# Performance work log

Measured on AMD Instinct MI355X. Metric: run time of the kernel, lower is better.

## Reference

```python
import jax, jax.numpy as jnp
import numpy as np

N_NODES = 50000
N_EDGES = 625000
D_IN, D_HID, D_OUT = 512, 128, 1


def gcn_conv(x, W, b, src, dst, n_nodes):
    """PyG GCNConv: add self-loops, symmetric D^-1/2 (A+I) D^-1/2 normalization.
    x: [N, d_in], W: [d_in, d_out], b: [d_out], src/dst: [E] int.
    """
    xw = x @ W  # [N, d_out] - linear before propagation (PyG order)
    # degree including self-loop
    deg = jax.ops.segment_sum(jnp.ones_like(src, dtype=xw.dtype), dst,
                              num_segments=n_nodes) + 1.0
    dinv = jax.lax.rsqrt(deg)  # [N]
    norm = dinv[src] * dinv[dst]  # [E]
    # neighbor aggregation (scatter-add over destination nodes)
    agg = jax.ops.segment_sum(xw[src] * norm[:, None], dst, num_segments=n_nodes)
    # self-loop contribution: norm_ii = dinv_i^2
    agg = agg + xw * (dinv * dinv)[:, None]
    return agg + b


def layer_norm(x, gamma, beta, eps=1e-5):
    mu = jnp.mean(x, axis=-1, keepdims=True)
    var = jnp.var(x, axis=-1, keepdims=True)
    return (x - mu) * jax.lax.rsqrt(var + eps) * gamma + beta


def setup_inputs() -> dict:
    key = jax.random.key(0)
    ks = jax.random.split(key, 12)
    x = jax.random.normal(ks[0], (N_NODES, D_IN), dtype=jnp.float32)
    edge_index = jax.random.randint(ks[1], (2, N_EDGES), 0, N_NODES, dtype=jnp.int64)

    def glorot(k, shape):
        lim = np.sqrt(6.0 / (shape[0] + shape[1]))
        return jax.random.uniform(k, shape, jnp.float32, -lim, lim)

    return {
        "x": x,
        "W1": glorot(ks[2], (D_IN, D_HID)), "b1": jnp.zeros((D_HID,), jnp.float32),
        "gamma1": jnp.ones((D_HID,), jnp.float32), "beta1": jnp.zeros((D_HID,), jnp.float32),
        "W2": glorot(ks[3], (D_HID, D_HID)), "b2": jnp.zeros((D_HID,), jnp.float32),
        "W3": glorot(ks[4], (D_HID, D_HID)), "b3": jnp.zeros((D_HID,), jnp.float32),
        "W4": glorot(ks[5], (D_HID, D_OUT)), "b4": jnp.zeros((D_OUT,), jnp.float32),
        "edge_index": edge_index,
    }


def reference(x, W1, b1, gamma1, beta1, W2, b2, W3, b3, W4, b4, edge_index):
    # eval mode: F.dropout(training=False) is identity
    src, dst = edge_index[0], edge_index[1]
    n = x.shape[0]
    h = jax.nn.relu(layer_norm(gcn_conv(x, W1, b1, src, dst, n), gamma1, beta1))
    h = jax.nn.relu(gcn_conv(h, W2, b2, src, dst, n))
    h = jax.nn.relu(gcn_conv(h, W3, b3, src, dst, n))
    h = gcn_conv(h, W4, b4, src, dst, n)
    return jnp.squeeze(h, axis=-1)  # [N]
```

## Files before the change

### kernel.cpp

```cpp
#include <hip/hip_runtime.h>
#include <hip/hip_bf16.h>
#include <cstdint>

#define D_IN 512
#define D_HID 128

typedef unsigned short u16;
typedef unsigned int u32;
typedef __attribute__((ext_vector_type(8))) short short8;
typedef __attribute__((ext_vector_type(4))) float f32x4;

__device__ __forceinline__ u16 f2bf(float f) {
    u32 u = __float_as_uint(f);
    u = (u + 0x7FFFu + ((u >> 16) & 1u)) >> 16;
    return (u16)u;
}
__device__ __forceinline__ float bfc(short x) {
    return __uint_as_float(((u32)(u16)x) << 16);
}

__global__ __launch_bounds__(256) void k_deg_int(const int* __restrict__ dst,
                                                 int* __restrict__ deg, int E) {
    int e = blockIdx.x * 256 + threadIdx.x;
    if (e < E) atomicAdd(&deg[dst[e]], 1);
}

__global__ __launch_bounds__(256) void k_scan_block(const int* __restrict__ deg,
                                                    int* __restrict__ rowptr,
                                                    int* __restrict__ bsum, int N) {
    __shared__ int sh[256];
    int i = blockIdx.x * 256 + threadIdx.x;
    int v = (i < N) ? deg[i] : 0;
    sh[threadIdx.x] = v;
    __syncthreads();
#pragma unroll
    for (int off = 1; off < 256; off <<= 1) {
        int t = (threadIdx.x >= off) ? sh[threadIdx.x - off] : 0;
        __syncthreads();
        sh[threadIdx.x] += t;
        __syncthreads();
    }
    int incl = sh[threadIdx.x];
    if (i < N) rowptr[i] = incl - v;
    if (threadIdx.x == 255) bsum[blockIdx.x] = incl;
}

__global__ __launch_bounds__(256) void k_apply_offset(int* __restrict__ rowptr,
                                                      const int* __restrict__ bsum,
                                                      int* __restrict__ deg_cursor,
                                                      float* __restrict__ dinv,
                                                      int N, int E, int P) {
    __shared__ int sh[256];
    int v = (threadIdx.x < P) ? bsum[threadIdx.x] : 0;
    sh[threadIdx.x] = v;
    __syncthreads();
#pragma unroll
    for (int off = 1; off < 256; off <<= 1) {
        int t = (threadIdx.x >= off) ? sh[threadIdx.x - off] : 0;
        __syncthreads();
        sh[threadIdx.x] += t;
        __syncthreads();
    }
    int boff = (blockIdx.x == 0) ? 0 : sh[blockIdx.x - 1];
    int i = blockIdx.x * 256 + threadIdx.x;
    if (i == 0) rowptr[N] = E;
    if (i >= N) return;
    int dv = deg_cursor[i];
    int rp = rowptr[i] + boff;
    rowptr[i] = rp;
    deg_cursor[i] = rp;
    dinv[i] = rsqrtf((float)dv + 1.0f);
}

__global__ __launch_bounds__(256) void k_fill_csr(const int* __restrict__ src,
                                                  const int* __restrict__ dst,
                                                  int* __restrict__ cursor,
                                                  int* __restrict__ csr, int E) {
    int e = blockIdx.x * 256 + threadIdx.x;
    if (e >= E) return;
    int pos = atomicAdd(&cursor[dst[e]], 1);
    csr[pos] = src[e];
}

__global__ __launch_bounds__(256) void k_wt_all(const float* __restrict__ W1,
                                                const float* __restrict__ W2,
                                                const float* __restrict__ W3,
                                                u16* __restrict__ WT1,
                                                u16* __restrict__ WT2,
                                                u16* __restrict__ WT3) {
    int t = blockIdx.x * 256 + threadIdx.x;
    if (t < 65536) {
        int c = t >> 9, k = t & 511;
        WT1[t] = f2bf(W1[(size_t)k * 128 + c]);
    } else if (t < 65536 + 16384) {
        int u = t - 65536;
        int c = u >> 7, k = u & 127;
        WT2[u] = f2bf(W2[(size_t)k * 128 + c]);
    } else if (t < 65536 + 32768) {
        int u = t - 65536 - 16384;
        int c = u >> 7, k = u & 127;
        WT3[u] = f2bf(W3[(size_t)k * 128 + c]);
    }
}

template <int K, typename TI>
__global__ __launch_bounds__(256) void k_gemm_mfma(const TI* __restrict__ X,
                                                   const u16* __restrict__ WT,
                                                   const float* __restrict__ dinv,
                                                   u16* __restrict__ Y, int N) {
    __shared__ u16 Xs[64 * 40];
    __shared__ u16 Ws[128 * 40];
    const int tid = threadIdx.x;
    const int wv = tid >> 6;
    const int lane = tid & 63;
    const int row0 = blockIdx.x * 64;
    const int rsel = lane & 15;
    const int kgrp = (lane >> 4) * 8;

    f32x4 acc[8];
#pragma unroll
    for (int c = 0; c < 8; ++c) acc[c] = (f32x4){0.f, 0.f, 0.f, 0.f};

    for (int k0 = 0; k0 < K; k0 += 32) {
        {
            int r = tid >> 2;
            int kk = (tid & 3) * 8;
            int row = row0 + r;
            if constexpr (sizeof(TI) == 4) {
                float v[8];
                if (row < N) {
                    float4 p0 = *(const float4*)&X[(size_t)row * K + k0 + kk];
                    float4 p1 = *(const float4*)&X[(size_t)row * K + k0 + kk + 4];
                    v[0] = p0.x; v[1] = p0.y; v[2] = p0.z; v[3] = p0.w;
                    v[4] = p1.x; v[5] = p1.y; v[6] = p1.z; v[7] = p1.w;
                } else {
#pragma unroll
                    for (int i = 0; i < 8; ++i) v[i] = 0.f;
                }
                union { u16 us[8]; short8 v8; } tmp;
#pragma unroll
                for (int i = 0; i < 8; ++i) tmp.us[i] = f2bf(v[i]);
                *(short8*)&Xs[r * 40 + kk] = tmp.v8;
            } else {
                short8 v8 = {};
                if (row < N) v8 = *(const short8*)&X[(size_t)row * K + k0 + kk];
                *(short8*)&Xs[r * 40 + kk] = v8;
            }
        }
        {
            int col = tid >> 1;
            int kh = (tid & 1) * 16;
            const u16* g = &WT[(size_t)col * K + k0 + kh];
            u16* d = &Ws[col * 40 + kh];
            *(short8*)d = *(const short8*)g;
            *(short8*)(d + 8) = *(const short8*)(g + 8);
        }
        __syncthreads();
        short8 a = *(const short8*)&Xs[(wv * 16 + rsel) * 40 + kgrp];
#pragma unroll
        for (int c = 0; c < 8; ++c) {
            short8 b = *(const short8*)&Ws[(c * 16 + rsel) * 40 + kgrp];
            acc[c] = __builtin_amdgcn_mfma_f32_16x16x32_bf16(a, b, acc[c], 0, 0, 0);
        }
        __syncthreads();
    }
#pragma unroll
    for (int r = 0; r < 4; ++r) {
        int row = row0 + wv * 16 + (lane >> 4) * 4 + r;
        if (row < N) {
            float ds = dinv[row];
#pragma unroll
            for (int c = 0; c < 8; ++c)
                Y[(size_t)row * 128 + c * 16 + rsel] = f2bf(acc[c][r] * ds);
        }
    }
}

#define GATHER_CORE(XW, rowptr, csr, node, q, es, a)                               \
    int beg = rowptr[node], end = rowptr[node + 1];                                \
    float a[8];                                                                    \
    _Pragma("unroll") for (int i = 0; i < 8; ++i) a[i] = 0.f;                      \
    {                                                                              \
        int j = beg + es;                                                          \
        for (; j + 12 < end; j += 16) {                                            \
            int s0 = csr[j], s1 = csr[j + 4], s2 = csr[j + 8], s3 = csr[j + 12];   \
            short8 r0 = *(const short8*)&XW[(size_t)s0 * 128 + q * 8];             \
            short8 r1 = *(const short8*)&XW[(size_t)s1 * 128 + q * 8];             \
            short8 r2 = *(const short8*)&XW[(size_t)s2 * 128 + q * 8];             \
            short8 r3 = *(const short8*)&XW[(size_t)s3 * 128 + q * 8];             \
            _Pragma("unroll") for (int i = 0; i < 8; ++i)                          \
                a[i] += (bfc(r0[i]) + bfc(r1[i])) + (bfc(r2[i]) + bfc(r3[i]));     \
        }                                                                          \
        if (j + 4 < end) {                                                         \
            int s0 = csr[j], s1 = csr[j + 4];                                      \
            short8 r0 = *(const short8*)&XW[(size_t)s0 * 128 + q * 8];             \
            short8 r1 = *(const short8*)&XW[(size_t)s1 * 128 + q * 8];             \
            _Pragma("unroll") for (int i = 0; i < 8; ++i)                          \
                a[i] += bfc(r0[i]) + bfc(r1[i]);                                   \
            j += 8;                                                                \
        }                                                                          \
        if (j < end) {                                                             \
            int s = csr[j];                                                        \
            short8 r = *(const short8*)&XW[(size_t)s * 128 + q * 8];               \
            _Pragma("unroll") for (int i = 0; i < 8; ++i) a[i] += bfc(r[i]);       \
        }                                                                          \
    }                                                                              \
    _Pragma("unroll") for (int i = 0; i < 8; ++i) {                                \
        a[i] += __shfl_xor(a[i], 16);                                              \
        a[i] += __shfl_xor(a[i], 32);                                              \
    }

__global__ __launch_bounds__(256) void k_gather_ln_relu(const u16* __restrict__ XW,
                                                        const int* __restrict__ rowptr,
                                                        const int* __restrict__ csr,
                                                        const float* __restrict__ dinv,
                                                        const float* __restrict__ b,
                                                        const float* __restrict__ gamma,
                                                        const float* __restrict__ beta,
                                                        u16* __restrict__ H, int N) {
    int node = blockIdx.x * 4 + (threadIdx.x >> 6);
    int lane = threadIdx.x & 63;
    int q = lane & 15;
    int es = lane >> 4;
    if (node >= N) return;
    float di = dinv[node];
    GATHER_CORE(XW, rowptr, csr, node, q, es, a)
    short8 us = *(const short8*)&XW[(size_t)node * 128 + q * 8];
    float4 b0 = *(const float4*)&b[q * 8];
    float4 b1 = *(const float4*)&b[q * 8 + 4];
    float v[8];
#pragma unroll
    for (int i = 0; i < 8; ++i) {
        float bb = (i < 4) ? ((const float*)&b0)[i] : ((const float*)&b1)[i - 4];
        v[i] = (a[i] + bfc(us[i])) * di + bb;
    }
    float s = 0.f, sq = 0.f;
#pragma unroll
    for (int i = 0; i < 8; ++i) { s += v[i]; sq += v[i] * v[i]; }
#pragma unroll
    for (int off = 8; off; off >>= 1) {
        s  += __shfl_xor(s, off);
        sq += __shfl_xor(sq, off);
    }
    float mu  = s * (1.f / 128.f);
    float var = sq * (1.f / 128.f) - mu * mu;
    float rr  = rsqrtf(var + 1e-5f);
    float4 g0 = *(const float4*)&gamma[q * 8];
    float4 g1 = *(const float4*)&gamma[q * 8 + 4];
    float4 e0 = *(const float4*)&beta[q * 8];
    float4 e1 = *(const float4*)&beta[q * 8 + 4];
    if (es == 0) {
        union { u16 us[8]; short8 v8; } o;
#pragma unroll
        for (int i = 0; i < 8; ++i) {
            float gg = (i < 4) ? ((const float*)&g0)[i] : ((const float*)&g1)[i - 4];
            float ee = (i < 4) ? ((const float*)&e0)[i] : ((const float*)&e1)[i - 4];
            o.us[i] = f2bf(fmaxf((v[i] - mu) * rr * gg + ee, 0.f));
        }
        *(short8*)&H[(size_t)node * 128 + q * 8] = o.v8;
    }
}

__global__ __launch_bounds__(256) void k_gather_relu(const u16* __restrict__ XW,
                                                     const int* __restrict__ rowptr,
                                                     const int* __restrict__ csr,
                                                     const float* __restrict__ dinv,
                                                     const float* __restrict__ b,
                                                     u16* __restrict__ H, int N) {
    int node = blockIdx.x * 4 + (threadIdx.x >> 6);
    int lane = threadIdx.x & 63;
    int q = lane & 15;
    int es = lane >> 4;
    if (node >= N) return;
    float di = dinv[node];
    GATHER_CORE(XW, rowptr, csr, node, q, es, a)
    if (es != 0) return;
    short8 us = *(const short8*)&XW[(size_t)node * 128 + q * 8];
    float4 b0 = *(const float4*)&b[q * 8];
    float4 b1 = *(const float4*)&b[q * 8 + 4];
    union { u16 us[8]; short8 v8; } o;
#pragma unroll
    for (int i = 0; i < 8; ++i) {
        float bb = (i < 4) ? ((const float*)&b0)[i] : ((const float*)&b1)[i - 4];
        o.us[i] = f2bf(fmaxf((a[i] + bfc(us[i])) * di + bb, 0.f));
    }
    *(short8*)&H[(size_t)node * 128 + q * 8] = o.v8;
}

__global__ __launch_bounds__(256) void k_gather_dot(const u16* __restrict__ XW,
                                                    const int* __restrict__ rowptr,
                                                    const int* __restrict__ csr,
                                                    const float* __restrict__ dinv,
                                                    const float* __restrict__ b,
                                                    const float* __restrict__ W4,
                                                    float* __restrict__ XW4, int N) {
    int node = blockIdx.x * 4 + (threadIdx.x >> 6);
    int lane = threadIdx.x & 63;
    int q = lane & 15;
    int es = lane >> 4;
    if (node >= N) return;
    float di = dinv[node];
    GATHER_CORE(XW, rowptr, csr, node, q, es, a)
    short8 us = *(const short8*)&XW[(size_t)node * 128 + q * 8];
    float4 b0 = *(const float4*)&b[q * 8];
    float4 b1 = *(const float4*)&b[q * 8 + 4];
    float4 w0 = *(const float4*)&W4[q * 8];
    float4 w1 = *(const float4*)&W4[q * 8 + 4];
    float t = 0.f;
#pragma unroll
    for (int i = 0; i < 8; ++i) {
        float bb = (i < 4) ? ((const float*)&b0)[i] : ((const float*)&b1)[i - 4];
        float ww = (i < 4) ? ((const float*)&w0)[i] : ((const float*)&w1)[i - 4];
        float v = fmaxf((a[i] + bfc(us[i])) * di + bb, 0.f);
        t += v * ww;
    }
#pragma unroll
    for (int off = 8; off; off >>= 1) t += __shfl_xor(t, off);
    if (lane == 0) XW4[node] = t * di;
}

__global__ __launch_bounds__(256) void k_final_scalar(const float* __restrict__ XW4,
                                                      const int* __restrict__ rowptr,
                                                      const int* __restrict__ csr,
                                                      const float* __restrict__ dinv,
                                                      const float* __restrict__ b4,
                                                      float* __restrict__ OUT, int N) {
    int node = blockIdx.x * 16 + (threadIdx.x >> 4);
    int q = threadIdx.x & 15;
    if (node >= N) return;
    int beg = rowptr[node], end = rowptr[node + 1];
    float acc = 0.f;
    for (int j = beg + q; j < end; j += 16) {
        acc += XW4[csr[j]];
    }
#pragma unroll
    for (int off = 8; off; off >>= 1) acc += __shfl_xor(acc, off);
    if (q == 0) {
        OUT[node] = dinv[node] * (acc + XW4[node]) + b4[0];
    }
}

static inline size_t alignup(size_t x) { return (x + 255) & ~(size_t)255; }

extern "C" void kernel_launch(void* const* d_in, const int* in_sizes, int n_in,
                              void* d_out, int out_size, void* d_ws, size_t ws_size,
                              hipStream_t stream) {
    const float* x      = (const float*)d_in[0];
    const float* W1     = (const float*)d_in[1];
    const float* b1     = (const float*)d_in[2];
    const float* gamma1 = (const float*)d_in[3];
    const float* beta1  = (const float*)d_in[4];
    const float* W2     = (const float*)d_in[5];
    const float* b2     = (const float*)d_in[6];
    const float* W3     = (const float*)d_in[7];
    const float* b3     = (const float*)d_in[8];
    const float* W4     = (const float*)d_in[9];
    const float* b4     = (const float*)d_in[10];
    const int*   ei     = (const int*)d_in[11];

    const int N = in_sizes[0] / D_IN;
    const int E = in_sizes[11] / 2;
    const int* src = ei;
    const int* dst = ei + E;

    char* ws = (char*)d_ws;
    size_t off = 0;
    int*   deg_cur = (int*)(ws + off);   off += alignup((size_t)N * 4);
    int*   rowptr  = (int*)(ws + off);   off += alignup((size_t)(N + 1) * 4);
    int*   bsum    = (int*)(ws + off);   off += alignup(256 * 4);
    float* dinv    = (float*)(ws + off); off += alignup((size_t)N * 4);
    float* xw4     = (float*)(ws + off); off += alignup((size_t)N * 4);
    int*   csr     = (int*)(ws + off);   off += alignup((size_t)E * 4);
    u16*   WT1     = (u16*)(ws + off);   off += alignup((size_t)128 * 512 * 2);
    u16*   WT2     = (u16*)(ws + off);   off += alignup((size_t)128 * 128 * 2);
    u16*   WT3     = (u16*)(ws + off);   off += alignup((size_t)128 * 128 * 2);
    u16*   XW      = (u16*)(ws + off);   off += alignup((size_t)N * 128 * 2);
    u16*   H       = (u16*)(ws + off);

    const int scanBlocks = (N + 255) / 256;

    hipMemsetAsync(deg_cur, 0, (size_t)N * 4, stream);
    k_deg_int<<<(E + 255) / 256, 256, 0, stream>>>(dst, deg_cur, E);
    k_scan_block<<<scanBlocks, 256, 0, stream>>>(deg_cur, rowptr, bsum, N);
    k_apply_offset<<<scanBlocks, 256, 0, stream>>>(rowptr, bsum, deg_cur, dinv,
                                                   N, E, scanBlocks);
    k_fill_csr<<<(E + 255) / 256, 256, 0, stream>>>(src, dst, deg_cur, csr, E);

    k_wt_all<<<(65536 + 32768 + 255) / 256, 256, 0, stream>>>(W1, W2, W3, WT1, WT2, WT3);

    const int gemmGrid   = (N + 63) / 64;
    const int gatherGrid = (N + 3) / 4;

    k_gemm_mfma<512, float><<<gemmGrid, 256, 0, stream>>>(x, WT1, dinv, XW, N);
    k_gather_ln_relu<<<gatherGrid, 256, 0, stream>>>(XW, rowptr, csr, dinv,
                                                     b1, gamma1, beta1, H, N);
    k_gemm_mfma<128, u16><<<gemmGrid, 256, 0, stream>>>(H, WT2, dinv, XW, N);
    k_gather_relu<<<gatherGrid, 256, 0, stream>>>(XW, rowptr, csr, dinv, b2, H, N);
    k_gemm_mfma<128, u16><<<gemmGrid, 256, 0, stream>>>(H, WT3, dinv, XW, N);
    k_gather_dot<<<gatherGrid, 256, 0, stream>>>(XW, rowptr, csr, dinv, b3, W4, xw4, N);
    k_final_scalar<<<(N + 15) / 16, 256, 0, stream>>>(xw4, rowptr, csr, dinv,
                                                      b4, (float*)d_out, N);
}
```

Measured before the change: 374.2 us.

## Store layer-2 GEMM output in column chunks and gather per chunk

The second GEMM now writes its output in four column-chunked planes of 32 features each, and the layer-2 gather kernel is replaced by one that launches four blocks per node group, each aggregating only one 64-byte chunk. The aim is to shrink the working set of each gather pass so that random neighbor reads hit in cache more often. The cost is four times as many blocks, each rereading the CSR indices, plus narrower 4-byte loads and scattered 2-byte stores from the GEMM epilogue.

```diff
diff --git a/kernel.cpp b/kernel.cpp
--- a/kernel.cpp
+++ b/kernel.cpp
@@ -18,6 +18,8 @@
 __device__ __forceinline__ float bfc(short x) {
     return __uint_as_float(((u32)(u16)x) << 16);
 }
+__device__ __forceinline__ float bflo(u32 u) { return __uint_as_float(u << 16); }
+__device__ __forceinline__ float bfhi(u32 u) { return __uint_as_float(u & 0xFFFF0000u); }
 
 __global__ __launch_bounds__(256) void k_deg_int(const int* __restrict__ dst,
                                                  int* __restrict__ deg, int E) {
@@ -103,7 +105,7 @@
     }
 }
 
-template <int K, typename TI>
+template <int K, typename TI, bool CHUNKED>
 __global__ __launch_bounds__(256) void k_gemm_mfma(const TI* __restrict__ X,
                                                    const u16* __restrict__ WT,
                                                    const float* __restrict__ dinv,
@@ -170,8 +172,15 @@
         if (row < N) {
             float ds = dinv[row];
 #pragma unroll
-            for (int c = 0; c < 8; ++c)
-                Y[(size_t)row * 128 + c * 16 + rsel] = f2bf(acc[c][r] * ds);
+            for (int c = 0; c < 8; ++c) {
+                u16 val = f2bf(acc[c][r] * ds);
+                if constexpr (CHUNKED) {
+                    int col = c * 16 + rsel;
+                    Y[((size_t)(col >> 5) * N + row) * 32 + (col & 31)] = val;
+                } else {
+                    Y[(size_t)row * 128 + c * 16 + rsel] = val;
+                }
+            }
         }
     }
 }
@@ -261,30 +270,57 @@
     }
 }
 
-__global__ __launch_bounds__(256) void k_gather_relu(const u16* __restrict__ XW,
-                                                     const int* __restrict__ rowptr,
-                                                     const int* __restrict__ csr,
-                                                     const float* __restrict__ dinv,
-                                                     const float* __restrict__ b,
-                                                     u16* __restrict__ H, int N) {
-    int node = blockIdx.x * 4 + (threadIdx.x >> 6);
+__global__ __launch_bounds__(256) void k_gather_relu_ch(const u16* __restrict__ XWc,
+                                                        const int* __restrict__ rowptr,
+                                                        const int* __restrict__ csr,
+                                                        const float* __restrict__ dinv,
+                                                        const float* __restrict__ b,
+                                                        u16* __restrict__ H, int N) {
+    int bid = blockIdx.x;
+    int chunk = bid & 3;
+    int node = ((bid >> 2) << 2) + (threadIdx.x >> 6);
     int lane = threadIdx.x & 63;
     int q = lane & 15;
     int es = lane >> 4;
     if (node >= N) return;
     float di = dinv[node];
-    GATHER_CORE(XW, rowptr, csr, node, q, es, a)
+    const u16* XW = XWc + (size_t)chunk * N * 32;
+    int beg = rowptr[node], end = rowptr[node + 1];
+    float a0 = 0.f, a1 = 0.f;
+    {
+        int j = beg + es;
+        for (; j + 12 < end; j += 16) {
+            int s0 = csr[j], s1 = csr[j + 4], s2 = csr[j + 8], s3 = csr[j + 12];
+            u32 r0 = *(const u32*)&XW[(size_t)s0 * 32 + q * 2];
+            u32 r1 = *(const u32*)&XW[(size_t)s1 * 32 + q * 2];
+            u32 r2 = *(const u32*)&XW[(size_t)s2 * 32 + q * 2];
+            u32 r3 = *(const u32*)&XW[(size_t)s3 * 32 + q * 2];
+            a0 += (bflo(r0) + bflo(r1)) + (bflo(r2) + bflo(r3));
+            a1 += (bfhi(r0) + bfhi(r1)) + (bfhi(r2) + bfhi(r3));
+        }
+        if (j + 4 < end) {
+            int s0 = csr[j], s1 = csr[j + 4];
+            u32 r0 = *(const u32*)&XW[(size_t)s0 * 32 + q * 2];
+            u32 r1 = *(const u32*)&XW[(size_t)s1 * 32 + q * 2];
+            a0 += bflo(r0) + bflo(r1);
+            a1 += bfhi(r0) + bfhi(r1);
+            j += 8;
+        }
+        if (j < end) {
+            int s = csr[j];
+            u32 r = *(const u32*)&XW[(size_t)s * 32 + q * 2];
+            a0 += bflo(r);
+            a1 += bfhi(r);
+        }
+    }
+    a0 += __shfl_xor(a0, 16); a0 += __shfl_xor(a0, 32);
+    a1 += __shfl_xor(a1, 16); a1 += __shfl_xor(a1, 32);
     if (es != 0) return;
-    short8 us = *(const short8*)&XW[(size_t)node * 128 + q * 8];
-    float4 b0 = *(const float4*)&b[q * 8];
-    float4 b1 = *(const float4*)&b[q * 8 + 4];
-    union { u16 us[8]; short8 v8; } o;
-#pragma unroll
-    for (int i = 0; i < 8; ++i) {
-        float bb = (i < 4) ? ((const float*)&b0)[i] : ((const float*)&b1)[i - 4];
-        o.us[i] = f2bf(fmaxf((a[i] + bfc(us[i])) * di + bb, 0.f));
-    }
-    *(short8*)&H[(size_t)node * 128 + q * 8] = o.v8;
+    u32 us = *(const u32*)&XW[(size_t)node * 32 + q * 2];
+    float2 bb = *(const float2*)&b[chunk * 32 + q * 2];
+    u32 o0 = f2bf(fmaxf((a0 + bflo(us)) * di + bb.x, 0.f));
+    u32 o1 = f2bf(fmaxf((a1 + bfhi(us)) * di + bb.y, 0.f));
+    *(u32*)&H[(size_t)node * 128 + chunk * 32 + q * 2] = (o1 << 16) | o0;
 }
 
 __global__ __launch_bounds__(256) void k_gather_dot(const u16* __restrict__ XW,
@@ -390,13 +426,14 @@
 
     const int gemmGrid   = (N + 63) / 64;
     const int gatherGrid = (N + 3) / 4;
-
-    k_gemm_mfma<512, float><<<gemmGrid, 256, 0, stream>>>(x, WT1, dinv, XW, N);
+    const int chunkGrid  = ((N + 3) / 4) * 4;
+
+    k_gemm_mfma<512, float, false><<<gemmGrid, 256, 0, stream>>>(x, WT1, dinv, XW, N);
     k_gather_ln_relu<<<gatherGrid, 256, 0, stream>>>(XW, rowptr, csr, dinv,
                                                      b1, gamma1, beta1, H, N);
-    k_gemm_mfma<128, u16><<<gemmGrid, 256, 0, stream>>>(H, WT2, dinv, XW, N);
-    k_gather_relu<<<gatherGrid, 256, 0, stream>>>(XW, rowptr, csr, dinv, b2, H, N);
-    k_gemm_mfma<128, u16><<<gemmGrid, 256, 0, stream>>>(H, WT3, dinv, XW, N);
+    k_gemm_mfma<128, u16, true><<<gemmGrid, 256, 0, stream>>>(H, WT2, dinv, XW, N);
+    k_gather_relu_ch<<<chunkGrid, 256, 0, stream>>>(XW, rowptr, csr, dinv, b2, H, N);
+    k_gemm_mfma<128, u16, false><<<gemmGrid, 256, 0, stream>>>(H, WT3, dinv, XW, N);
     k_gather_dot<<<gatherGrid, 256, 0, stream>>>(XW, rowptr, csr, dinv, b3, W4, xw4, N);
     k_final_scalar<<<(N + 15) / 16, 256, 0, stream>>>(xw4, rowptr, csr, dinv,
                                                       b4, (float*)d_out, N);
```

Result: slower. 419.2 us (+12.0%).
